# Kernel optimization log

Hardware: AMD Instinct MI355X
Metric: run time of the kernel (lower is better)

## Reference

```python
import jax, jax.numpy as jnp
import numpy as np

B = 1024      # batch
DIN = 103     # generator/encoder input dim
L1, L2 = 64, 32   # encoder layer widths (latent = 32)
E = 8         # NUM_EXPERTS
GH = 64       # gating hidden width
H = 256       # generator hidden width
DOUT = 51     # generator output dim
EPS = 1e-5    # BatchNorm eps


def setup_inputs() -> dict:
    key = jax.random.key(0)
    ks = jax.random.split(key, 24)
    s = 0.05
    f32 = jnp.float32
    return {
        "x": jax.random.normal(ks[0], (B, DIN), f32),
        # encoder Linear + BN params
        "w1": jax.random.normal(ks[1], (L1, DIN), f32) * s,
        "b1": jnp.zeros((L1,), f32),
        "gamma1": jnp.ones((L1,), f32),
        "beta1": jnp.zeros((L1,), f32),
        "w2": jax.random.normal(ks[2], (L2, L1), f32) * s,
        "b2": jnp.zeros((L2,), f32),
        "gamma2": jnp.ones((L2,), f32),
        "beta2": jnp.zeros((L2,), f32),
        # gating MLP (latent 32 -> GH -> GH -> E, ELU, softmax)
        "gw1": jax.random.normal(ks[3], (GH, L2), f32) * s,
        "gb1": jnp.zeros((GH,), f32),
        "gw2": jax.random.normal(ks[4], (GH, GH), f32) * s,
        "gb2": jnp.zeros((GH,), f32),
        "gw3": jax.random.normal(ks[5], (E, GH), f32) * s,
        "gb3": jnp.zeros((E,), f32),
        # expert weight banks for 3-layer generator (MANN style)
        "ew1": jax.random.normal(ks[6], (E, DIN, H), f32) * s,
        "eb1": jnp.zeros((E, H), f32),
        "ew2": jax.random.normal(ks[7], (E, H, H), f32) * s,
        "eb2": jnp.zeros((E, H), f32),
        "ew3": jax.random.normal(ks[8], (E, H, DOUT), f32) * s,
        "eb3": jnp.zeros((E, DOUT), f32),
    }


def _batchnorm(h, gamma, beta):
    # training-mode BatchNorm1d: per-batch mean/var (biased var, matching torch)
    m = jnp.mean(h, axis=0)
    v = jnp.mean((h - m) ** 2, axis=0)
    return gamma * (h - m) * jax.lax.rsqrt(v + EPS) + beta


def reference(x, w1, b1, gamma1, beta1, w2, b2, gamma2, beta2,
              gw1, gb1, gw2, gb2, gw3, gb3,
              ew1, eb1, ew2, eb2, ew3, eb3):
    # in-place scale of last 3 features (x[:,100:103] *= 100)
    xs = x.at[:, 100:103].multiply(100.0)
    # encoder: Linear -> BN -> ReLU, twice
    h = jax.nn.relu(_batchnorm(xs @ w1.T + b1, gamma1, beta1))
    latent = jax.nn.relu(_batchnorm(h @ w2.T + b2, gamma2, beta2))
    # gating network -> blending coefficients BC [B, E]
    g = jax.nn.elu(latent @ gw1.T + gb1)
    g = jax.nn.elu(g @ gw2.T + gb2)
    bc = jax.nn.softmax(g @ gw3.T + gb3, axis=-1)
    # MANN-style generator: per-sample expert-blended weights
    wb1 = jnp.einsum('be,eih->bih', bc, ew1)   # [B, DIN, H]
    h1 = jax.nn.elu(jnp.einsum('bi,bih->bh', xs, wb1) + bc @ eb1)
    wb2 = jnp.einsum('be,ehk->bhk', bc, ew2)   # [B, H, H]
    h2 = jax.nn.elu(jnp.einsum('bh,bhk->bk', h1, wb2) + bc @ eb2)
    wb3 = jnp.einsum('be,eho->bho', bc, ew3)   # [B, H, DOUT]
    out = jnp.einsum('bh,bho->bo', h2, wb3) + bc @ eb3
    return out
```

## Files before the change

### kernel.cpp

```cpp
#include <hip/hip_runtime.h>
#include <math.h>


#define DIN 103
#define NE  8
#define HH  256
#define DOUT 51
#define EPSBN 1e-5f

typedef __attribute__((ext_vector_type(8))) short bf16x8;
typedef __attribute__((ext_vector_type(4))) float f32x4;
typedef __attribute__((ext_vector_type(8))) unsigned short us8;
typedef unsigned short ushort_t;

__device__ __forceinline__ float eluf(float v) { return v > 0.f ? v : (expf(v) - 1.f); }
__device__ __forceinline__ unsigned short bf16h(float f) {
  unsigned u = __float_as_uint(f);
  u += 0x7FFFu + ((u >> 16) & 1u);
  return (unsigned short)(u >> 16);
}
__device__ __forceinline__ float bf16f(unsigned short h) { return __uint_as_float(((unsigned)h) << 16); }
__device__ __forceinline__ void split_bf16(float v, unsigned short& h, unsigned short& l) {
  h = bf16h(v);
  l = bf16h(v - bf16f(h));
}
#define MFMA __builtin_amdgcn_mfma_f32_16x16x32_bf16

__device__ __forceinline__ void stA(float* p, float v) {
  __hip_atomic_store(p, v, __ATOMIC_RELAXED, __HIP_MEMORY_SCOPE_AGENT);
}
__device__ __forceinline__ float ldA(const float* p) {
  return __hip_atomic_load((float*)p, __ATOMIC_RELAXED, __HIP_MEMORY_SCOPE_AGENT);
}
__device__ __forceinline__ void stAu(unsigned* p, unsigned v) {
  __hip_atomic_store(p, v, __ATOMIC_RELAXED, __HIP_MEMORY_SCOPE_AGENT);
}
__device__ __forceinline__ unsigned ldAu(const unsigned* p) {
  return __hip_atomic_load((unsigned*)p, __ATOMIC_RELAXED, __HIP_MEMORY_SCOPE_AGENT);
}

#define O_SLOTS1 0
#define O_SLOTS2 8192
#define O_H1RAW  20480
#define O_XSH    118784
#define O_XSL    184320
#define O_E1H    258048
#define O_E1L    389120
#define O_E2H    520192
#define O_E3H    782336
#define O_ESPAN  589824
#define O_BAR    1372160

__device__ __forceinline__ void gbar64(unsigned* base, int blk) {
  asm volatile("s_waitcnt vmcnt(0)" ::: "memory");
  __syncthreads();
  if (threadIdx.x == 0) {
    unsigned a = __hip_atomic_fetch_add(base + (blk >> 3) * 32, 1u,
                                        __ATOMIC_RELAXED, __HIP_MEMORY_SCOPE_AGENT);
    if (a == 7u) {
      unsigned r = __hip_atomic_fetch_add(base + 256, 1u,
                                          __ATOMIC_RELAXED, __HIP_MEMORY_SCOPE_AGENT);
      if (r == 7u) {
#pragma unroll
        for (int j = 0; j < 8; ++j) stAu(base + 288 + j * 32, 1u);
      }
    }
    while (ldAu(base + 288 + (blk & 7) * 32) == 0u)
      __builtin_amdgcn_s_sleep(2);
  }
  __syncthreads();
}

__global__ __launch_bounds__(256) void k_prep_enc1(
    const float* __restrict__ x, const float* __restrict__ w1, const float* __restrict__ b1,
    const float* __restrict__ ew1, const float* __restrict__ ew2, const float* __restrict__ ew3,
    float* __restrict__ ws) {
  __shared__ union {
    float tile[32][65];
    float xt[16][104];
    struct { float w1L[64 * DIN]; float xr[16][104]; float hb[16][64]; } e1;
  } sm;
  int bk = blockIdx.x, t = threadIdx.x;
  int l2 = t & 63, c = l2 & 15, q = l2 >> 4;
  if (bk == 0) {
    unsigned* bz = (unsigned*)(ws + O_BAR);
#pragma unroll
    for (int i = 0; i < 4; ++i) bz[t + i * 256] = 0u;
  }

  if (bk < 256) {
    int nh = bk & 3, kc = (bk >> 2) & 7, e = bk >> 5;
    int k0 = kc * 32, n0 = nh * 64;
#pragma unroll
    for (int i = 0; i < 8; ++i) {
      int kl = (t >> 6) + i * 4;
      sm.tile[kl][t & 63] = ew2[((size_t)e * HH + k0 + kl) * HH + n0 + (t & 63)];
    }
    __syncthreads();
    int nsl = t >> 6;
    us8 H8;
#pragma unroll
    for (int j = 0; j < 8; ++j) H8[j] = bf16h(sm.tile[q * 8 + j][nsl * 16 + c]);
    size_t dst = (((size_t)(e * 16 + nh * 4 + nsl)) * 8 + kc) * 512 + l2 * 8;
    *(us8*)((ushort_t*)(ws + O_E2H) + dst) = H8;
  } else if (bk < 384) {
    int b2 = bk - 256;
    int nh = b2 & 3, kc = (b2 >> 2) & 3, e = b2 >> 4;
    int k0 = kc * 32, n0 = nh * 64;
#pragma unroll
    for (int i = 0; i < 8; ++i) {
      int kl = (t >> 6) + i * 4;
      int k = k0 + kl;
      sm.tile[kl][t & 63] = (k < DIN) ? ew1[((size_t)e * DIN + k) * HH + n0 + (t & 63)] : 0.f;
    }
    __syncthreads();
    int nsl = t >> 6;
    us8 H8, L8;
#pragma unroll
    for (int j = 0; j < 8; ++j) {
      unsigned short h, lo; split_bf16(sm.tile[q * 8 + j][nsl * 16 + c], h, lo);
      H8[j] = h; L8[j] = lo;
    }
    size_t dst = (((size_t)(e * 16 + nh * 4 + nsl)) * 4 + kc) * 512 + l2 * 8;
    *(us8*)((ushort_t*)(ws + O_E1H) + dst) = H8;
    *(us8*)((ushort_t*)(ws + O_E1L) + dst) = L8;
  } else if (bk < 448) {
    int b2 = bk - 384;
    int kc = b2 & 7, e = b2 >> 3;
    int k0 = kc * 32;
#pragma unroll
    for (int i = 0; i < 8; ++i) {
      int kl = (t >> 6) + i * 4;
      int n = t & 63;
      sm.tile[kl][n] = (n < DOUT) ? ew3[((size_t)e * HH + k0 + kl) * DOUT + n] : 0.f;
    }
    __syncthreads();
    int nsl = t >> 6;
    us8 H8;
#pragma unroll
    for (int j = 0; j < 8; ++j) H8[j] = bf16h(sm.tile[q * 8 + j][nsl * 16 + c]);
    size_t dst = (((size_t)(e * 4 + nsl)) * 8 + kc) * 512 + l2 * 8;
    *(us8*)((ushort_t*)(ws + O_E3H) + dst) = H8;
  } else if (bk < 512) {
    int msub = bk - 448;
    for (int i = t; i < 16 * 104; i += 256) {
      int b = i / 104, k = i - b * 104;
      float v = 0.f;
      if (k < DIN) { v = x[(size_t)(msub * 16 + b) * DIN + k]; if (k >= 100) v *= 100.f; }
      sm.xt[b][k] = v;
    }
    __syncthreads();
    int kc = t >> 6;
    int m = c;
    us8 H8, L8;
#pragma unroll
    for (int j = 0; j < 8; ++j) {
      int k = kc * 32 + q * 8 + j;
      float v = (k < 104) ? sm.xt[m][k] : 0.f;
      unsigned short h, lo; split_bf16(v, h, lo);
      H8[j] = h; L8[j] = lo;
    }
    size_t dst = ((size_t)msub * 4 + kc) * 512 + l2 * 8;
    *(us8*)((ushort_t*)(ws + O_XSH) + dst) = H8;
    *(us8*)((ushort_t*)(ws + O_XSL) + dst) = L8;
  } else {
    float* slots1 = ws + O_SLOTS1;
    float* h1raw  = ws + O_H1RAW;
    int bkl = bk - 512;
    int r0 = bkl * 16;
    for (int i = t; i < 64 * DIN; i += 256) sm.e1.w1L[i] = w1[i];
    for (int i = t; i < 16 * 104; i += 256) {
      int r = i / 104, c2 = i - r * 104;
      float v = 0.f;
      if (c2 < DIN) { v = x[(size_t)(r0 + r) * DIN + c2]; if (c2 >= 100) v *= 100.f; }
      sm.e1.xr[r][c2] = v;
    }
    __syncthreads();
#pragma unroll
    for (int i = 0; i < 4; ++i) {
      int idx = t + i * 256;
      int r = idx >> 6, j = idx & 63;
      float acc = b1[j];
      for (int k = 0; k < DIN; ++k) acc = fmaf(sm.e1.xr[r][k], sm.e1.w1L[j * DIN + k], acc);
      sm.e1.hb[r][j] = acc;
      h1raw[(size_t)(r0 + r) * 64 + j] = acc;
    }
    __syncthreads();
    if (t < 64) {
      float s = 0.f, qq = 0.f;
      for (int r = 0; r < 16; ++r) { float v = sm.e1.hb[r][t]; s += v; qq += v * v; }
      slots1[bkl * 128 + t] = s;
      slots1[bkl * 128 + 64 + t] = qq;
    }
  }
}

__global__ __launch_bounds__(512) void k_mega(
    const float* __restrict__ gamma1, const float* __restrict__ beta1,
    const float* __restrict__ w2, const float* __restrict__ b2,
    const float* __restrict__ gamma2, const float* __restrict__ beta2,
    const float* __restrict__ gw1, const float* __restrict__ gb1,
    const float* __restrict__ gw2, const float* __restrict__ gb2,
    const float* __restrict__ gw3, const float* __restrict__ gb3,
    const float* __restrict__ eb1, const float* __restrict__ eb2,
    const float* __restrict__ eb3,
    float* __restrict__ ws, float* __restrict__ out) {
  __shared__ union {
    struct { float w2T[64 * 33]; float red[128]; float sc1[64], sh1[64];
             float h1b[16][64]; } enc2;
    struct { float gw1L[64 * 33]; float gw2L[64 * 65]; float gw3L[8 * 65];
             float gb1L[64], gb2L[64], gb3L[8];
             float red2[64], sc2[32], sh2[32];
             float lat[16][32]; float g1[16][64], g2[16][64]; } gate;
    struct { float hT[256][17]; float eb[2048]; } comb;
    struct { float p3s[8][16][64]; float eb3L[8][64]; } g3;
  } U;
  __shared__ float hb2s[16][32];
  __shared__ us8 aHv[512], aLv[512];
  __shared__ float bcL[16][8];

  const int blk = blockIdx.x, t = threadIdx.x;
  const int wv = t >> 6, l = t & 63, c = l & 15, quad = l >> 4;
  const int R0 = blk * 16;
  unsigned* bar = (unsigned*)(ws + O_BAR);
  const ushort_t* XsH = (const ushort_t*)(ws + O_XSH);
  const ushort_t* XsL = (const ushort_t*)(ws + O_XSL);
  const ushort_t* E1H = (const ushort_t*)(ws + O_E1H);
  const ushort_t* E1L = (const ushort_t*)(ws + O_E1L);
  const ushort_t* E2H = (const ushort_t*)(ws + O_E2H);
  const ushort_t* E3H = (const ushort_t*)(ws + O_E3H);

  bf16x8 a1h[4], a1l[4];
#pragma unroll
  for (int kc = 0; kc < 4; ++kc) {
    a1h[kc] = *(const bf16x8*)(XsH + ((size_t)blk * 4 + kc) * 512 + l * 8);
    a1l[kc] = *(const bf16x8*)(XsL + ((size_t)blk * 4 + kc) * 512 + l * 8);
  }

  {
    const int slice = blk >> 3;
    const float4* src = (const float4*)(ws + O_E1H);
    float ka = 0.f;
#pragma unroll
    for (int i = 0; i < 36; ++i) {
      float4 v = src[(size_t)slice * 18432 + (size_t)i * 512 + t];
      ka += v.x + v.y + v.z + v.w;
    }
    asm volatile("" :: "v"(ka));
  }

  {
    const float* slots1 = ws + O_SLOTS1;
    float* slots2 = ws + O_SLOTS2;
    const float* h1raw = ws + O_H1RAW;
    for (int i = t; i < 2048; i += 512) { int j = i >> 6, k = i & 63; U.enc2.w2T[k * 33 + j] = w2[i]; }
    if (t < 128) {
      float s = 0.f;
      for (int b = 0; b < 64; ++b) s += slots1[b * 128 + t];
      U.enc2.red[t] = s;
    }
    __syncthreads();
    if (t < 64) {
      float mm = U.enc2.red[t] * (1.f / 1024.f);
      float v = U.enc2.red[64 + t] * (1.f / 1024.f) - mm * mm;
      float sc = gamma1[t] * rsqrtf(v + EPSBN);
      U.enc2.sc1[t] = sc; U.enc2.sh1[t] = beta1[t] - mm * sc;
    }
    __syncthreads();
#pragma unroll
    for (int i = 0; i < 2; ++i) {
      int idx = t + i * 512;
      int r = idx >> 6, k = idx & 63;
      U.enc2.h1b[r][k] = fmaxf(fmaf(h1raw[(size_t)(R0 + r) * 64 + k], U.enc2.sc1[k], U.enc2.sh1[k]), 0.f);
    }
    __syncthreads();
    {
      int r = t >> 5, j = t & 31;
      float acc = b2[j];
      for (int k = 0; k < 64; ++k) acc = fmaf(U.enc2.h1b[r][k], U.enc2.w2T[k * 33 + j], acc);
      hb2s[r][j] = acc;
    }
    __syncthreads();
    if (t < 32) {
      float s = 0.f, q = 0.f;
      for (int r = 0; r < 16; ++r) { float v = hb2s[r][t]; s += v; q += v * v; }
      stA(slots2 + blk * 64 + t, s);
      stA(slots2 + blk * 64 + 32 + t, q);
    }
  }
  gbar64(bar, blk);

  {
    const float* slots2 = ws + O_SLOTS2;
    for (int i = t; i < 2048; i += 512) { int j = i >> 5, k = i & 31; U.gate.gw1L[j * 33 + k] = gw1[i]; }
    for (int i = t; i < 4096; i += 512) { int j = i >> 6, k = i & 63; U.gate.gw2L[j * 65 + k] = gw2[i]; }
    { int j = t >> 6, k = t & 63; U.gate.gw3L[j * 65 + k] = gw3[t]; }
    if (t < 64) { U.gate.gb1L[t] = gb1[t]; U.gate.gb2L[t] = gb2[t]; }
    if (t < 8) U.gate.gb3L[t] = gb3[t];
    if (t < 64) {
      float vvv[64];
#pragma unroll
      for (int b = 0; b < 64; ++b) vvv[b] = ldA(slots2 + b * 64 + t);
      float s = 0.f;
#pragma unroll
      for (int b = 0; b < 64; ++b) s += vvv[b];
      U.gate.red2[t] = s;
    }
    __syncthreads();
    if (t < 32) {
      float mm = U.gate.red2[t] * (1.f / 1024.f);
      float v = U.gate.red2[32 + t] * (1.f / 1024.f) - mm * mm;
      float sc = gamma2[t] * rsqrtf(v + EPSBN);
      U.gate.sc2[t] = sc; U.gate.sh2[t] = beta2[t] - mm * sc;
    }
    __syncthreads();
    { int r = t >> 5, cc = t & 31;
      U.gate.lat[r][cc] = fmaxf(fmaf(hb2s[r][cc], U.gate.sc2[cc], U.gate.sh2[cc]), 0.f); }
    __syncthreads();
#pragma unroll
    for (int rr = 0; rr < 2; ++rr) {
      int r = wv * 2 + rr;
      float a1 = U.gate.gb1L[l];
      for (int k = 0; k < 32; ++k) a1 = fmaf(U.gate.gw1L[l * 33 + k], U.gate.lat[r][k], a1);
      U.gate.g1[r][l] = eluf(a1);
    }
    __syncthreads();
#pragma unroll
    for (int rr = 0; rr < 2; ++rr) {
      int r = wv * 2 + rr;
      float a2 = U.gate.gb2L[l];
      for (int k = 0; k < 64; ++k) a2 = fmaf(U.gate.gw2L[l * 65 + k], U.gate.g1[r][k], a2);
      U.gate.g2[r][l] = eluf(a2);
    }
    __syncthreads();
#pragma unroll
    for (int rr = 0; rr < 2; ++rr) {
      int r = wv * 2 + rr;
      if (l < 8) {
        float a3 = U.gate.gb3L[l];
        for (int k = 0; k < 64; ++k) a3 = fmaf(U.gate.gw3L[l * 65 + k], U.gate.g2[r][k], a3);
        float mx = a3;
        mx = fmaxf(mx, __shfl_xor(mx, 1));
        mx = fmaxf(mx, __shfl_xor(mx, 2));
        mx = fmaxf(mx, __shfl_xor(mx, 4));
        float p = expf(a3 - mx);
        float sp = p;
        sp += __shfl_xor(sp, 1); sp += __shfl_xor(sp, 2); sp += __shfl_xor(sp, 4);
        bcL[r][l] = p / sp;
      }
    }
    __syncthreads();

    for (int i = t; i < 2048; i += 512) U.comb.eb[i] = eb1[i];
    __syncthreads();
    {
      f32x4 blend[2] = {};
#pragma unroll
      for (int e = 0; e < NE; ++e) {
        float bcv[4];
#pragma unroll
        for (int r = 0; r < 4; ++r) bcv[r] = bcL[quad * 4 + r][e];
#pragma unroll
        for (int nsi = 0; nsi < 2; ++nsi) {
          int ns = wv * 2 + nsi;
          f32x4 acc = {};
#pragma unroll
          for (int kc = 0; kc < 4; ++kc) {
            size_t bo = (((size_t)(e * 16 + ns)) * 4 + kc) * 512 + l * 8;
            bf16x8 bh = *(const bf16x8*)(E1H + bo);
            bf16x8 bl = *(const bf16x8*)(E1L + bo);
            acc = MFMA(a1h[kc], bh, acc, 0, 0, 0);
            acc = MFMA(a1l[kc], bh, acc, 0, 0, 0);
            acc = MFMA(a1h[kc], bl, acc, 0, 0, 0);
          }
          float ebv = U.comb.eb[e * HH + ns * 16 + c];
#pragma unroll
          for (int r = 0; r < 4; ++r) blend[nsi][r] = fmaf(bcv[r], acc[r] + ebv, blend[nsi][r]);
        }
      }
#pragma unroll
      for (int nsi = 0; nsi < 2; ++nsi) {
        int col = (wv * 2 + nsi) * 16 + c;
#pragma unroll
        for (int r = 0; r < 4; ++r) U.comb.hT[col][quad * 4 + r] = eluf(blend[nsi][r]);
      }
    }
    __syncthreads();
    {
      int l2 = t & 63, row = l2 & 15, k0 = (t >> 6) * 32 + (l2 >> 4) * 8;
      us8 H, L;
#pragma unroll
      for (int j = 0; j < 8; ++j) {
        unsigned short h, lo; split_bf16(U.comb.hT[k0 + j][row], h, lo);
        H[j] = h; L[j] = lo;
      }
      aHv[t] = H; aLv[t] = L;
    }
    __syncthreads();
  }

  {
    for (int i = t; i < 2048; i += 512) U.comb.eb[i] = eb2[i];
    bf16x8 a2h[8], a2l[8];
#pragma unroll
    for (int kc = 0; kc < 8; ++kc) {
      a2h[kc] = *(const bf16x8*)&aHv[kc * 64 + l];
      a2l[kc] = *(const bf16x8*)&aLv[kc * 64 + l];
    }
    __syncthreads();
    {
      f32x4 blend[2] = {};
#pragma unroll
      for (int e = 0; e < NE; ++e) {
        float bcv[4];
#pragma unroll
        for (int r = 0; r < 4; ++r) bcv[r] = bcL[quad * 4 + r][e];
#pragma unroll
        for (int nsi = 0; nsi < 2; ++nsi) {
          int ns = wv * 2 + nsi;
          f32x4 acc = {};
#pragma unroll
          for (int kc = 0; kc < 8; ++kc) {
            size_t bo = (((size_t)(e * 16 + ns)) * 8 + kc) * 512 + l * 8;
            bf16x8 bh = *(const bf16x8*)(E2H + bo);
            acc = MFMA(a2h[kc], bh, acc, 0, 0, 0);
            acc = MFMA(a2l[kc], bh, acc, 0, 0, 0);
          }
          float ebv = U.comb.eb[e * HH + ns * 16 + c];
#pragma unroll
          for (int r = 0; r < 4; ++r) blend[nsi][r] = fmaf(bcv[r], acc[r] + ebv, blend[nsi][r]);
        }
      }
#pragma unroll
      for (int nsi = 0; nsi < 2; ++nsi) {
        int col = (wv * 2 + nsi) * 16 + c;
#pragma unroll
        for (int r = 0; r < 4; ++r) U.comb.hT[col][quad * 4 + r] = eluf(blend[nsi][r]);
      }
    }
    __syncthreads();
    {
      int l2 = t & 63, row = l2 & 15, k0 = (t >> 6) * 32 + (l2 >> 4) * 8;
      us8 H, L;
#pragma unroll
      for (int j = 0; j < 8; ++j) {
        unsigned short h, lo; split_bf16(U.comb.hT[k0 + j][row], h, lo);
        H[j] = h; L[j] = lo;
      }
      aHv[t] = H; aLv[t] = L;
    }
    __syncthreads();
  }

  {
    { int e = t >> 6, n = t & 63; U.g3.eb3L[e][n] = (n < DOUT) ? eb3[e * DOUT + n] : 0.f; }
    const int e = wv;
    f32x4 acc[4] = {};
#pragma unroll
    for (int kc = 0; kc < 8; ++kc) {
      bf16x8 ah = *(const bf16x8*)&aHv[kc * 64 + l];
      bf16x8 al = *(const bf16x8*)&aLv[kc * 64 + l];
#pragma unroll
      for (int nsi = 0; nsi < 4; ++nsi) {
        size_t bo = (((size_t)(e * 4 + nsi)) * 8 + kc) * 512 + l * 8;
        bf16x8 bh = *(const bf16x8*)(E3H + bo);
        acc[nsi] = MFMA(ah, bh, acc[nsi], 0, 0, 0);
        acc[nsi] = MFMA(al, bh, acc[nsi], 0, 0, 0);
      }
    }
#pragma unroll
    for (int nsi = 0; nsi < 4; ++nsi)
#pragma unroll
      for (int r = 0; r < 4; ++r)
        U.g3.p3s[e][quad * 4 + r][nsi * 16 + c] = acc[nsi][r];
    __syncthreads();
#pragma unroll
    for (int i = 0; i < 2; ++i) {
      int idx = t + i * 512;
      int row = idx >> 6, col = idx & 63;
      float s = 0.f;
#pragma unroll
      for (int e2 = 0; e2 < 8; ++e2)
        s = fmaf(bcL[row][e2], U.g3.p3s[e2][row][col] + U.g3.eb3L[e2][col], s);
      if (col < DOUT) out[(size_t)(R0 + row) * DOUT + col] = s;
    }
  }
}

extern "C" void kernel_launch(void* const* d_in, const int* in_sizes, int n_in,
                              void* d_out, int out_size, void* d_ws, size_t ws_size,
                              hipStream_t stream) {
  const float* x      = (const float*)d_in[0];
  const float* w1     = (const float*)d_in[1];
  const float* b1     = (const float*)d_in[2];
  const float* gamma1 = (const float*)d_in[3];
  const float* beta1  = (const float*)d_in[4];
  const float* w2     = (const float*)d_in[5];
  const float* b2     = (const float*)d_in[6];
  const float* gamma2 = (const float*)d_in[7];
  const float* beta2  = (const float*)d_in[8];
  const float* gw1    = (const float*)d_in[9];
  const float* gb1    = (const float*)d_in[10];
  const float* gw2    = (const float*)d_in[11];
  const float* gb2    = (const float*)d_in[12];
  const float* gw3    = (const float*)d_in[13];
  const float* gb3    = (const float*)d_in[14];
  const float* ew1    = (const float*)d_in[15];
  const float* eb1    = (const float*)d_in[16];
  const float* ew2    = (const float*)d_in[17];
  const float* eb2    = (const float*)d_in[18];
  const float* ew3    = (const float*)d_in[19];
  const float* eb3    = (const float*)d_in[20];
  float* wsf  = (float*)d_ws;
  float* outp = (float*)d_out;

  k_prep_enc1<<<576, 256, 0, stream>>>(x, w1, b1, ew1, ew2, ew3, wsf);
  k_mega<<<64, 512, 0, stream>>>(gamma1, beta1, w2, b2, gamma2, beta2,
                                 gw1, gb1, gw2, gb2, gw3, gb3,
                                 eb1, eb2, eb3, wsf, outp);
}
```

Before: 151.2 us.

## Double k_mega block to 1024 threads, one wave per output column tile

Launches the persistent mega-kernel with 1024 threads (16 waves) per block instead of 512, and reassigns work so that each wave handles one 16-column tile in the layer-1 and layer-2 blended MFMA loops instead of two. The gating MLP now gives one row per wave, and the layer-3 expert MFMAs are restricted to the first 8 waves. The aim is more latency hiding and parallelism within each of the 64 blocks on a grid that is otherwise small. In exchange, register pressure is higher at 1024 launch bounds, and the A-operand fragments for layer 2 are reloaded from memory inside the loop rather than kept in registers.

Result: faster. 141.9 us (-6.1%).

```diff
diff --git a/kernel.cpp b/kernel.cpp
--- a/kernel.cpp
+++ b/kernel.cpp
@@ -48,7 +48,6 @@
 #define O_E1L    389120
 #define O_E2H    520192
 #define O_E3H    782336
-#define O_ESPAN  589824
 #define O_BAR    1372160
 
 __device__ __forceinline__ void gbar64(unsigned* base, int blk) {
@@ -195,7 +194,7 @@
   }
 }
 
-__global__ __launch_bounds__(512) void k_mega(
+__global__ __launch_bounds__(1024) void k_mega(
     const float* __restrict__ gamma1, const float* __restrict__ beta1,
     const float* __restrict__ w2, const float* __restrict__ b2,
     const float* __restrict__ gamma2, const float* __restrict__ beta2,
@@ -242,8 +241,8 @@
     const float4* src = (const float4*)(ws + O_E1H);
     float ka = 0.f;
 #pragma unroll
-    for (int i = 0; i < 36; ++i) {
-      float4 v = src[(size_t)slice * 18432 + (size_t)i * 512 + t];
+    for (int i = 0; i < 18; ++i) {
+      float4 v = src[(size_t)slice * 18432 + (size_t)i * 1024 + t];
       ka += v.x + v.y + v.z + v.w;
     }
     asm volatile("" :: "v"(ka));
@@ -253,7 +252,7 @@
     const float* slots1 = ws + O_SLOTS1;
     float* slots2 = ws + O_SLOTS2;
     const float* h1raw = ws + O_H1RAW;
-    for (int i = t; i < 2048; i += 512) { int j = i >> 6, k = i & 63; U.enc2.w2T[k * 33 + j] = w2[i]; }
+    for (int i = t; i < 2048; i += 1024) { int j = i >> 6, k = i & 63; U.enc2.w2T[k * 33 + j] = w2[i]; }
     if (t < 128) {
       float s = 0.f;
       for (int b = 0; b < 64; ++b) s += slots1[b * 128 + t];
@@ -267,14 +266,10 @@
       U.enc2.sc1[t] = sc; U.enc2.sh1[t] = beta1[t] - mm * sc;
     }
     __syncthreads();
-#pragma unroll
-    for (int i = 0; i < 2; ++i) {
-      int idx = t + i * 512;
-      int r = idx >> 6, k = idx & 63;
-      U.enc2.h1b[r][k] = fmaxf(fmaf(h1raw[(size_t)(R0 + r) * 64 + k], U.enc2.sc1[k], U.enc2.sh1[k]), 0.f);
-    }
-    __syncthreads();
-    {
+    { int r = t >> 6, k = t & 63;
+      U.enc2.h1b[r][k] = fmaxf(fmaf(h1raw[(size_t)(R0 + r) * 64 + k], U.enc2.sc1[k], U.enc2.sh1[k]), 0.f); }
+    __syncthreads();
+    if (t < 512) {
       int r = t >> 5, j = t & 31;
       float acc = b2[j];
       for (int k = 0; k < 64; ++k) acc = fmaf(U.enc2.h1b[r][k], U.enc2.w2T[k * 33 + j], acc);
@@ -292,9 +287,9 @@
 
   {
     const float* slots2 = ws + O_SLOTS2;
-    for (int i = t; i < 2048; i += 512) { int j = i >> 5, k = i & 31; U.gate.gw1L[j * 33 + k] = gw1[i]; }
-    for (int i = t; i < 4096; i += 512) { int j = i >> 6, k = i & 63; U.gate.gw2L[j * 65 + k] = gw2[i]; }
-    { int j = t >> 6, k = t & 63; U.gate.gw3L[j * 65 + k] = gw3[t]; }
+    for (int i = t; i < 2048; i += 1024) { int j = i >> 5, k = i & 31; U.gate.gw1L[j * 33 + k] = gw1[i]; }
+    for (int i = t; i < 4096; i += 1024) { int j = i >> 6, k = i & 63; U.gate.gw2L[j * 65 + k] = gw2[i]; }
+    if (t < 512) { int j = t >> 6, k = t & 63; U.gate.gw3L[j * 65 + k] = gw3[t]; }
     if (t < 64) { U.gate.gb1L[t] = gb1[t]; U.gate.gb2L[t] = gb2[t]; }
     if (t < 8) U.gate.gb3L[t] = gb3[t];
     if (t < 64) {
@@ -314,28 +309,22 @@
       U.gate.sc2[t] = sc; U.gate.sh2[t] = beta2[t] - mm * sc;
     }
     __syncthreads();
-    { int r = t >> 5, cc = t & 31;
+    if (t < 512) { int r = t >> 5, cc = t & 31;
       U.gate.lat[r][cc] = fmaxf(fmaf(hb2s[r][cc], U.gate.sc2[cc], U.gate.sh2[cc]), 0.f); }
     __syncthreads();
-#pragma unroll
-    for (int rr = 0; rr < 2; ++rr) {
-      int r = wv * 2 + rr;
+    { int r = wv;
       float a1 = U.gate.gb1L[l];
       for (int k = 0; k < 32; ++k) a1 = fmaf(U.gate.gw1L[l * 33 + k], U.gate.lat[r][k], a1);
       U.gate.g1[r][l] = eluf(a1);
     }
     __syncthreads();
-#pragma unroll
-    for (int rr = 0; rr < 2; ++rr) {
-      int r = wv * 2 + rr;
+    { int r = wv;
       float a2 = U.gate.gb2L[l];
       for (int k = 0; k < 64; ++k) a2 = fmaf(U.gate.gw2L[l * 65 + k], U.gate.g1[r][k], a2);
       U.gate.g2[r][l] = eluf(a2);
     }
     __syncthreads();
-#pragma unroll
-    for (int rr = 0; rr < 2; ++rr) {
-      int r = wv * 2 + rr;
+    { int r = wv;
       if (l < 8) {
         float a3 = U.gate.gb3L[l];
         for (int k = 0; k < 64; ++k) a3 = fmaf(U.gate.gw3L[l * 65 + k], U.gate.g2[r][k], a3);
@@ -351,42 +340,36 @@
     }
     __syncthreads();
 
-    for (int i = t; i < 2048; i += 512) U.comb.eb[i] = eb1[i];
+    for (int i = t; i < 2048; i += 1024) U.comb.eb[i] = eb1[i];
     __syncthreads();
     {
-      f32x4 blend[2] = {};
+      const int ns = wv;
+      f32x4 blend = {};
 #pragma unroll
       for (int e = 0; e < NE; ++e) {
         float bcv[4];
 #pragma unroll
         for (int r = 0; r < 4; ++r) bcv[r] = bcL[quad * 4 + r][e];
-#pragma unroll
-        for (int nsi = 0; nsi < 2; ++nsi) {
-          int ns = wv * 2 + nsi;
-          f32x4 acc = {};
-#pragma unroll
-          for (int kc = 0; kc < 4; ++kc) {
-            size_t bo = (((size_t)(e * 16 + ns)) * 4 + kc) * 512 + l * 8;
-            bf16x8 bh = *(const bf16x8*)(E1H + bo);
-            bf16x8 bl = *(const bf16x8*)(E1L + bo);
-            acc = MFMA(a1h[kc], bh, acc, 0, 0, 0);
-            acc = MFMA(a1l[kc], bh, acc, 0, 0, 0);
-            acc = MFMA(a1h[kc], bl, acc, 0, 0, 0);
-          }
-          float ebv = U.comb.eb[e * HH + ns * 16 + c];
-#pragma unroll
-          for (int r = 0; r < 4; ++r) blend[nsi][r] = fmaf(bcv[r], acc[r] + ebv, blend[nsi][r]);
+        f32x4 acc = {};
+#pragma unroll
+        for (int kc = 0; kc < 4; ++kc) {
+          size_t bo = (((size_t)(e * 16 + ns)) * 4 + kc) * 512 + l * 8;
+          bf16x8 bh = *(const bf16x8*)(E1H + bo);
+          bf16x8 bl = *(const bf16x8*)(E1L + bo);
+          acc = MFMA(a1h[kc], bh, acc, 0, 0, 0);
+          acc = MFMA(a1l[kc], bh, acc, 0, 0, 0);
+          acc = MFMA(a1h[kc], bl, acc, 0, 0, 0);
         }
-      }
-#pragma unroll
-      for (int nsi = 0; nsi < 2; ++nsi) {
-        int col = (wv * 2 + nsi) * 16 + c;
-#pragma unroll
-        for (int r = 0; r < 4; ++r) U.comb.hT[col][quad * 4 + r] = eluf(blend[nsi][r]);
-      }
-    }
-    __syncthreads();
-    {
+        float ebv = U.comb.eb[e * HH + ns * 16 + c];
+#pragma unroll
+        for (int r = 0; r < 4; ++r) blend[r] = fmaf(bcv[r], acc[r] + ebv, blend[r]);
+      }
+      int col = ns * 16 + c;
+#pragma unroll
+      for (int r = 0; r < 4; ++r) U.comb.hT[col][quad * 4 + r] = eluf(blend[r]);
+    }
+    __syncthreads();
+    if (t < 512) {
       int l2 = t & 63, row = l2 & 15, k0 = (t >> 6) * 32 + (l2 >> 4) * 8;
       us8 H, L;
 #pragma unroll
@@ -400,46 +383,36 @@
   }
 
   {
-    for (int i = t; i < 2048; i += 512) U.comb.eb[i] = eb2[i];
-    bf16x8 a2h[8], a2l[8];
-#pragma unroll
-    for (int kc = 0; kc < 8; ++kc) {
-      a2h[kc] = *(const bf16x8*)&aHv[kc * 64 + l];
-      a2l[kc] = *(const bf16x8*)&aLv[kc * 64 + l];
-    }
+    for (int i = t; i < 2048; i += 1024) U.comb.eb[i] = eb2[i];
     __syncthreads();
     {
-      f32x4 blend[2] = {};
+      const int ns = wv;
+      f32x4 blend = {};
 #pragma unroll
       for (int e = 0; e < NE; ++e) {
         float bcv[4];
 #pragma unroll
         for (int r = 0; r < 4; ++r) bcv[r] = bcL[quad * 4 + r][e];
-#pragma unroll
-        for (int nsi = 0; nsi < 2; ++nsi) {
-          int ns = wv * 2 + nsi;
-          f32x4 acc = {};
-#pragma unroll
-          for (int kc = 0; kc < 8; ++kc) {
-            size_t bo = (((size_t)(e * 16 + ns)) * 8 + kc) * 512 + l * 8;
-            bf16x8 bh = *(const bf16x8*)(E2H + bo);
-            acc = MFMA(a2h[kc], bh, acc, 0, 0, 0);
-            acc = MFMA(a2l[kc], bh, acc, 0, 0, 0);
-          }
-          float ebv = U.comb.eb[e * HH + ns * 16 + c];
-#pragma unroll
-          for (int r = 0; r < 4; ++r) blend[nsi][r] = fmaf(bcv[r], acc[r] + ebv, blend[nsi][r]);
+        f32x4 acc = {};
+#pragma unroll
+        for (int kc = 0; kc < 8; ++kc) {
+          size_t bo = (((size_t)(e * 16 + ns)) * 8 + kc) * 512 + l * 8;
+          bf16x8 bh = *(const bf16x8*)(E2H + bo);
+          bf16x8 ah = *(const bf16x8*)&aHv[kc * 64 + l];
+          bf16x8 al = *(const bf16x8*)&aLv[kc * 64 + l];
+          acc = MFMA(ah, bh, acc, 0, 0, 0);
+          acc = MFMA(al, bh, acc, 0, 0, 0);
         }
-      }
-#pragma unroll
-      for (int nsi = 0; nsi < 2; ++nsi) {
-        int col = (wv * 2 + nsi) * 16 + c;
-#pragma unroll
-        for (int r = 0; r < 4; ++r) U.comb.hT[col][quad * 4 + r] = eluf(blend[nsi][r]);
-      }
-    }
-    __syncthreads();
-    {
+        float ebv = U.comb.eb[e * HH + ns * 16 + c];
+#pragma unroll
+        for (int r = 0; r < 4; ++r) blend[r] = fmaf(bcv[r], acc[r] + ebv, blend[r]);
+      }
+      int col = ns * 16 + c;
+#pragma unroll
+      for (int r = 0; r < 4; ++r) U.comb.hT[col][quad * 4 + r] = eluf(blend[r]);
+    }
+    __syncthreads();
+    if (t < 512) {
       int l2 = t & 63, row = l2 & 15, k0 = (t >> 6) * 32 + (l2 >> 4) * 8;
       us8 H, L;
 #pragma unroll
@@ -453,31 +426,31 @@
   }
 
   {
-    { int e = t >> 6, n = t & 63; U.g3.eb3L[e][n] = (n < DOUT) ? eb3[e * DOUT + n] : 0.f; }
-    const int e = wv;
-    f32x4 acc[4] = {};
-#pragma unroll
-    for (int kc = 0; kc < 8; ++kc) {
-      bf16x8 ah = *(const bf16x8*)&aHv[kc * 64 + l];
-      bf16x8 al = *(const bf16x8*)&aLv[kc * 64 + l];
-#pragma unroll
-      for (int nsi = 0; nsi < 4; ++nsi) {
-        size_t bo = (((size_t)(e * 4 + nsi)) * 8 + kc) * 512 + l * 8;
-        bf16x8 bh = *(const bf16x8*)(E3H + bo);
-        acc[nsi] = MFMA(ah, bh, acc[nsi], 0, 0, 0);
-        acc[nsi] = MFMA(al, bh, acc[nsi], 0, 0, 0);
-      }
-    }
-#pragma unroll
-    for (int nsi = 0; nsi < 4; ++nsi)
-#pragma unroll
-      for (int r = 0; r < 4; ++r)
-        U.g3.p3s[e][quad * 4 + r][nsi * 16 + c] = acc[nsi][r];
-    __syncthreads();
-#pragma unroll
-    for (int i = 0; i < 2; ++i) {
-      int idx = t + i * 512;
-      int row = idx >> 6, col = idx & 63;
+    if (t < 512) { int e = t >> 6, n = t & 63; U.g3.eb3L[e][n] = (n < DOUT) ? eb3[e * DOUT + n] : 0.f; }
+    if (wv < 8) {
+      const int e = wv;
+      f32x4 acc[4] = {};
+#pragma unroll
+      for (int kc = 0; kc < 8; ++kc) {
+        bf16x8 ah = *(const bf16x8*)&aHv[kc * 64 + l];
+        bf16x8 al = *(const bf16x8*)&aLv[kc * 64 + l];
+#pragma unroll
+        for (int nsi = 0; nsi < 4; ++nsi) {
+          size_t bo = (((size_t)(e * 4 + nsi)) * 8 + kc) * 512 + l * 8;
+          bf16x8 bh = *(const bf16x8*)(E3H + bo);
+          acc[nsi] = MFMA(ah, bh, acc[nsi], 0, 0, 0);
+          acc[nsi] = MFMA(al, bh, acc[nsi], 0, 0, 0);
+        }
+      }
+#pragma unroll
+      for (int nsi = 0; nsi < 4; ++nsi)
+#pragma unroll
+        for (int r = 0; r < 4; ++r)
+          U.g3.p3s[e][quad * 4 + r][nsi * 16 + c] = acc[nsi][r];
+    }
+    __syncthreads();
+    {
+      int row = t >> 6, col = t & 63;
       float s = 0.f;
 #pragma unroll
       for (int e2 = 0; e2 < 8; ++e2)
@@ -515,7 +488,7 @@
   float* outp = (float*)d_out;
 
   k_prep_enc1<<<576, 256, 0, stream>>>(x, w1, b1, ew1, ew2, ew3, wsf);
-  k_mega<<<64, 512, 0, stream>>>(gamma1, beta1, w2, b2, gamma2, beta2,
-                                 gw1, gb1, gw2, gb2, gw3, gb3,
-                                 eb1, eb2, eb3, wsf, outp);
-}
+  k_mega<<<64, 1024, 0, stream>>>(gamma1, beta1, w2, b2, gamma2, beta2,
+                                  gw1, gb1, gw2, gb2, gw3, gb3,
+                                  eb1, eb2, eb3, wsf, outp);
+}
```

## Split generator layers across block groups with LDS-staged expert weights and grid barriers

Applied to the files above, without the earlier changes.

Each block used to compute all 256 hidden columns for its own 16 rows and read every expert weight tile straight from global memory. Now groups of four blocks share 64 rows. Each block computes one 64-column slice, and the expert weight tiles for that slice are staged in LDS once per expert and reused by all waves. Layer 1 and 2 activations, plus the blend coefficients, are exchanged through workspace buffers with three extra grid barriers. This cuts per-block weight traffic and drops the old L2 prefetch warm-up loop, at the cost of more grid-wide synchronisation and global round trips for activations.

Result: slower. 193.2 us (+27.8%).

```diff
diff --git a/kernel.cpp b/kernel.cpp
--- a/kernel.cpp
+++ b/kernel.cpp
@@ -38,9 +38,24 @@
 __device__ __forceinline__ unsigned ldAu(const unsigned* p) {
   return __hip_atomic_load((unsigned*)p, __ATOMIC_RELAXED, __HIP_MEMORY_SCOPE_AGENT);
 }
+union U16B { us8 v; bf16x8 b; unsigned u[4]; };
+__device__ __forceinline__ void st16A(void* p, us8 x) {
+  U16B t; t.v = x;
+  unsigned* d = (unsigned*)p;
+#pragma unroll
+  for (int j = 0; j < 4; ++j) stAu(d + j, t.u[j]);
+}
+__device__ __forceinline__ bf16x8 ld16A(const void* p) {
+  U16B t;
+  const unsigned* s = (const unsigned*)p;
+#pragma unroll
+  for (int j = 0; j < 4; ++j) t.u[j] = ldAu(s + j);
+  return t.b;
+}
 
 #define O_SLOTS1 0
 #define O_SLOTS2 8192
+#define O_BCG    12288
 #define O_H1RAW  20480
 #define O_XSH    118784
 #define O_XSL    184320
@@ -48,7 +63,10 @@
 #define O_E1L    389120
 #define O_E2H    520192
 #define O_E3H    782336
-#define O_ESPAN  589824
+#define O_A1H    847872
+#define O_A1L    978944
+#define O_A2H    1110016
+#define O_A2L    1241088
 #define O_BAR    1372160
 
 __device__ __forceinline__ void gbar64(unsigned* base, int blk) {
@@ -82,8 +100,8 @@
   } sm;
   int bk = blockIdx.x, t = threadIdx.x;
   int l2 = t & 63, c = l2 & 15, q = l2 >> 4;
-  if (bk == 0) {
-    unsigned* bz = (unsigned*)(ws + O_BAR);
+  if (bk < 4) {
+    unsigned* bz = (unsigned*)(ws + O_BAR) + bk * 1024;
 #pragma unroll
     for (int i = 0; i < 4; ++i) bz[t + i * 256] = 0u;
   }
@@ -212,41 +230,38 @@
              float gb1L[64], gb2L[64], gb3L[8];
              float red2[64], sc2[32], sh2[32];
              float lat[16][32]; float g1[16][64], g2[16][64]; } gate;
-    struct { float hT[256][17]; float eb[2048]; } comb;
+    struct { ushort_t stage[32 * 512]; float hT4[4][64][17]; float ebs[512]; } gen;
     struct { float p3s[8][16][64]; float eb3L[8][64]; } g3;
   } U;
   __shared__ float hb2s[16][32];
-  __shared__ us8 aHv[512], aLv[512];
-  __shared__ float bcL[16][8];
+  __shared__ float bc4L[4][16][8];
+  __shared__ float bcL2[16][8];
 
   const int blk = blockIdx.x, t = threadIdx.x;
   const int wv = t >> 6, l = t & 63, c = l & 15, quad = l >> 4;
-  const int R0 = blk * 16;
+  const int msub = blk;
+  const int R0 = msub * 16;
+  const int mg = blk >> 2, g = blk & 3;
+  const int ml = wv >> 1, nsp = wv & 1;
+  const int m_w = mg * 4 + ml;
   unsigned* bar = (unsigned*)(ws + O_BAR);
+  float* bcg = ws + O_BCG;
   const ushort_t* XsH = (const ushort_t*)(ws + O_XSH);
   const ushort_t* XsL = (const ushort_t*)(ws + O_XSL);
   const ushort_t* E1H = (const ushort_t*)(ws + O_E1H);
   const ushort_t* E1L = (const ushort_t*)(ws + O_E1L);
   const ushort_t* E2H = (const ushort_t*)(ws + O_E2H);
   const ushort_t* E3H = (const ushort_t*)(ws + O_E3H);
+  ushort_t* A1Hp = (ushort_t*)(ws + O_A1H);
+  ushort_t* A1Lp = (ushort_t*)(ws + O_A1L);
+  ushort_t* A2Hp = (ushort_t*)(ws + O_A2H);
+  ushort_t* A2Lp = (ushort_t*)(ws + O_A2L);
 
   bf16x8 a1h[4], a1l[4];
 #pragma unroll
   for (int kc = 0; kc < 4; ++kc) {
-    a1h[kc] = *(const bf16x8*)(XsH + ((size_t)blk * 4 + kc) * 512 + l * 8);
-    a1l[kc] = *(const bf16x8*)(XsL + ((size_t)blk * 4 + kc) * 512 + l * 8);
-  }
-
-  {
-    const int slice = blk >> 3;
-    const float4* src = (const float4*)(ws + O_E1H);
-    float ka = 0.f;
-#pragma unroll
-    for (int i = 0; i < 36; ++i) {
-      float4 v = src[(size_t)slice * 18432 + (size_t)i * 512 + t];
-      ka += v.x + v.y + v.z + v.w;
-    }
-    asm volatile("" :: "v"(ka));
+    a1h[kc] = *(const bf16x8*)(XsH + ((size_t)m_w * 4 + kc) * 512 + l * 8);
+    a1l[kc] = *(const bf16x8*)(XsL + ((size_t)m_w * 4 + kc) * 512 + l * 8);
   }
 
   {
@@ -284,8 +299,8 @@
     if (t < 32) {
       float s = 0.f, q = 0.f;
       for (int r = 0; r < 16; ++r) { float v = hb2s[r][t]; s += v; q += v * v; }
-      stA(slots2 + blk * 64 + t, s);
-      stA(slots2 + blk * 64 + 32 + t, q);
+      stA(slots2 + msub * 64 + t, s);
+      stA(slots2 + msub * 64 + 32 + t, q);
     }
   }
   gbar64(bar, blk);
@@ -346,126 +361,150 @@
         float p = expf(a3 - mx);
         float sp = p;
         sp += __shfl_xor(sp, 1); sp += __shfl_xor(sp, 2); sp += __shfl_xor(sp, 4);
-        bcL[r][l] = p / sp;
-      }
-    }
-    __syncthreads();
-
-    for (int i = t; i < 2048; i += 512) U.comb.eb[i] = eb1[i];
+        float bcv = p / sp;
+        bcL2[r][l] = bcv;
+        stA(bcg + (size_t)(R0 + r) * 8 + l, bcv);
+      }
+    }
+  }
+  gbar64(bar + 1024, blk);
+
+  {
+    { int mli = t >> 7, r = (t >> 3) & 15, e = t & 7;
+      bc4L[mli][r][e] = ldA(bcg + ((size_t)(mg * 4 + mli) * 16 + r) * 8 + e); }
+    { U.gen.ebs[t] = eb1[(t >> 6) * HH + g * 64 + (t & 63)]; }
+    f32x4 blend[2] = {};
+    for (int e = 0; e < 8; ++e) {
+      __syncthreads();
+#pragma unroll
+      for (int i = 0; i < 4; ++i) {
+        int s = wv * 4 + i;
+        int hl = s >> 4, nsl = (s >> 2) & 3, kc = s & 3;
+        const ushort_t* src = (hl ? E1L : E1H) + (((size_t)(e * 16 + g * 4 + nsl) * 4 + kc) * 512) + l * 8;
+        *(us8*)(U.gen.stage + s * 512 + l * 8) = *(const us8*)src;
+      }
+      __syncthreads();
+      float bcv[4];
+#pragma unroll
+      for (int r = 0; r < 4; ++r) bcv[r] = bc4L[ml][quad * 4 + r][e];
+#pragma unroll
+      for (int nsi = 0; nsi < 2; ++nsi) {
+        int nsl = nsp * 2 + nsi;
+        f32x4 acc = {};
+#pragma unroll
+        for (int kc = 0; kc < 4; ++kc) {
+          bf16x8 bh = *(const bf16x8*)(U.gen.stage + (size_t)((nsl * 4 + kc)) * 512 + l * 8);
+          bf16x8 bl = *(const bf16x8*)(U.gen.stage + (size_t)((16 + nsl * 4 + kc)) * 512 + l * 8);
+          acc = MFMA(a1h[kc], bh, acc, 0, 0, 0);
+          acc = MFMA(a1l[kc], bh, acc, 0, 0, 0);
+          acc = MFMA(a1h[kc], bl, acc, 0, 0, 0);
+        }
+        float ebv = U.gen.ebs[e * 64 + nsl * 16 + c];
+#pragma unroll
+        for (int r = 0; r < 4; ++r) blend[nsi][r] = fmaf(bcv[r], acc[r] + ebv, blend[nsi][r]);
+      }
+    }
+#pragma unroll
+    for (int nsi = 0; nsi < 2; ++nsi) {
+      int col = (nsp * 2 + nsi) * 16 + c;
+#pragma unroll
+      for (int r = 0; r < 4; ++r) U.gen.hT4[ml][col][quad * 4 + r] = eluf(blend[nsi][r]);
+    }
     __syncthreads();
     {
-      f32x4 blend[2] = {};
-#pragma unroll
-      for (int e = 0; e < NE; ++e) {
-        float bcv[4];
-#pragma unroll
-        for (int r = 0; r < 4; ++r) bcv[r] = bcL[quad * 4 + r][e];
-#pragma unroll
-        for (int nsi = 0; nsi < 2; ++nsi) {
-          int ns = wv * 2 + nsi;
-          f32x4 acc = {};
-#pragma unroll
-          for (int kc = 0; kc < 4; ++kc) {
-            size_t bo = (((size_t)(e * 16 + ns)) * 4 + kc) * 512 + l * 8;
-            bf16x8 bh = *(const bf16x8*)(E1H + bo);
-            bf16x8 bl = *(const bf16x8*)(E1L + bo);
-            acc = MFMA(a1h[kc], bh, acc, 0, 0, 0);
-            acc = MFMA(a1l[kc], bh, acc, 0, 0, 0);
-            acc = MFMA(a1h[kc], bl, acc, 0, 0, 0);
-          }
-          float ebv = U.comb.eb[e * HH + ns * 16 + c];
-#pragma unroll
-          for (int r = 0; r < 4; ++r) blend[nsi][r] = fmaf(bcv[r], acc[r] + ebv, blend[nsi][r]);
+      int mli = t >> 7, kcl = (t >> 6) & 1, l2 = t & 63, row = l2 & 15;
+      int k0l = kcl * 32 + (l2 >> 4) * 8;
+      us8 H, L;
+#pragma unroll
+      for (int j = 0; j < 8; ++j) {
+        unsigned short h, lo; split_bf16(U.gen.hT4[mli][k0l + j][row], h, lo);
+        H[j] = h; L[j] = lo;
+      }
+      size_t dst = ((size_t)(mg * 4 + mli) * 8 + g * 2 + kcl) * 512 + l2 * 8;
+      st16A(A1Hp + dst, H);
+      st16A(A1Lp + dst, L);
+    }
+  }
+  gbar64(bar + 2048, blk);
+
+  {
+    bf16x8 ah[8], al[8];
+#pragma unroll
+    for (int kc = 0; kc < 8; ++kc) {
+      ah[kc] = ld16A(A1Hp + ((size_t)m_w * 8 + kc) * 512 + l * 8);
+      al[kc] = ld16A(A1Lp + ((size_t)m_w * 8 + kc) * 512 + l * 8);
+    }
+    { U.gen.ebs[t] = eb2[(t >> 6) * HH + g * 64 + (t & 63)]; }
+    f32x4 blend[2] = {};
+    for (int e = 0; e < 8; ++e) {
+      __syncthreads();
+#pragma unroll
+      for (int i = 0; i < 4; ++i) {
+        int s = wv * 4 + i;
+        int nsl = s >> 3, kc = s & 7;
+        const ushort_t* src = E2H + (((size_t)(e * 16 + g * 4 + nsl) * 8 + kc) * 512) + l * 8;
+        *(us8*)(U.gen.stage + s * 512 + l * 8) = *(const us8*)src;
+      }
+      __syncthreads();
+      float bcv[4];
+#pragma unroll
+      for (int r = 0; r < 4; ++r) bcv[r] = bc4L[ml][quad * 4 + r][e];
+#pragma unroll
+      for (int nsi = 0; nsi < 2; ++nsi) {
+        int nsl = nsp * 2 + nsi;
+        f32x4 acc = {};
+#pragma unroll
+        for (int kc = 0; kc < 8; ++kc) {
+          bf16x8 bh = *(const bf16x8*)(U.gen.stage + (size_t)(nsl * 8 + kc) * 512 + l * 8);
+          acc = MFMA(ah[kc], bh, acc, 0, 0, 0);
+          acc = MFMA(al[kc], bh, acc, 0, 0, 0);
         }
-      }
-#pragma unroll
-      for (int nsi = 0; nsi < 2; ++nsi) {
-        int col = (wv * 2 + nsi) * 16 + c;
-#pragma unroll
-        for (int r = 0; r < 4; ++r) U.comb.hT[col][quad * 4 + r] = eluf(blend[nsi][r]);
-      }
+        float ebv = U.gen.ebs[e * 64 + nsl * 16 + c];
+#pragma unroll
+        for (int r = 0; r < 4; ++r) blend[nsi][r] = fmaf(bcv[r], acc[r] + ebv, blend[nsi][r]);
+      }
+    }
+#pragma unroll
+    for (int nsi = 0; nsi < 2; ++nsi) {
+      int col = (nsp * 2 + nsi) * 16 + c;
+#pragma unroll
+      for (int r = 0; r < 4; ++r) U.gen.hT4[ml][col][quad * 4 + r] = eluf(blend[nsi][r]);
     }
     __syncthreads();
     {
-      int l2 = t & 63, row = l2 & 15, k0 = (t >> 6) * 32 + (l2 >> 4) * 8;
+      int mli = t >> 7, kcl = (t >> 6) & 1, l2 = t & 63, row = l2 & 15;
+      int k0l = kcl * 32 + (l2 >> 4) * 8;
       us8 H, L;
 #pragma unroll
       for (int j = 0; j < 8; ++j) {
-        unsigned short h, lo; split_bf16(U.comb.hT[k0 + j][row], h, lo);
+        unsigned short h, lo; split_bf16(U.gen.hT4[mli][k0l + j][row], h, lo);
         H[j] = h; L[j] = lo;
       }
-      aHv[t] = H; aLv[t] = L;
-    }
-    __syncthreads();
-  }
-
-  {
-    for (int i = t; i < 2048; i += 512) U.comb.eb[i] = eb2[i];
-    bf16x8 a2h[8], a2l[8];
-#pragma unroll
-    for (int kc = 0; kc < 8; ++kc) {
-      a2h[kc] = *(const bf16x8*)&aHv[kc * 64 + l];
-      a2l[kc] = *(const bf16x8*)&aLv[kc * 64 + l];
-    }
-    __syncthreads();
-    {
-      f32x4 blend[2] = {};
-#pragma unroll
-      for (int e = 0; e < NE; ++e) {
-        float bcv[4];
-#pragma unroll
-        for (int r = 0; r < 4; ++r) bcv[r] = bcL[quad * 4 + r][e];
-#pragma unroll
-        for (int nsi = 0; nsi < 2; ++nsi) {
-          int ns = wv * 2 + nsi;
-          f32x4 acc = {};
-#pragma unroll
-          for (int kc = 0; kc < 8; ++kc) {
-            size_t bo = (((size_t)(e * 16 + ns)) * 8 + kc) * 512 + l * 8;
-            bf16x8 bh = *(const bf16x8*)(E2H + bo);
-            acc = MFMA(a2h[kc], bh, acc, 0, 0, 0);
-            acc = MFMA(a2l[kc], bh, acc, 0, 0, 0);
-          }
-          float ebv = U.comb.eb[e * HH + ns * 16 + c];
-#pragma unroll
-          for (int r = 0; r < 4; ++r) blend[nsi][r] = fmaf(bcv[r], acc[r] + ebv, blend[nsi][r]);
-        }
-      }
-#pragma unroll
-      for (int nsi = 0; nsi < 2; ++nsi) {
-        int col = (wv * 2 + nsi) * 16 + c;
-#pragma unroll
-        for (int r = 0; r < 4; ++r) U.comb.hT[col][quad * 4 + r] = eluf(blend[nsi][r]);
-      }
-    }
-    __syncthreads();
-    {
-      int l2 = t & 63, row = l2 & 15, k0 = (t >> 6) * 32 + (l2 >> 4) * 8;
-      us8 H, L;
-#pragma unroll
-      for (int j = 0; j < 8; ++j) {
-        unsigned short h, lo; split_bf16(U.comb.hT[k0 + j][row], h, lo);
-        H[j] = h; L[j] = lo;
-      }
-      aHv[t] = H; aLv[t] = L;
-    }
-    __syncthreads();
-  }
+      size_t dst = ((size_t)(mg * 4 + mli) * 8 + g * 2 + kcl) * 512 + l2 * 8;
+      st16A(A2Hp + dst, H);
+      st16A(A2Lp + dst, L);
+    }
+  }
+  gbar64(bar + 3072, blk);
 
   {
     { int e = t >> 6, n = t & 63; U.g3.eb3L[e][n] = (n < DOUT) ? eb3[e * DOUT + n] : 0.f; }
+    bf16x8 ah[8], al[8];
+#pragma unroll
+    for (int kc = 0; kc < 8; ++kc) {
+      ah[kc] = ld16A(A2Hp + ((size_t)msub * 8 + kc) * 512 + l * 8);
+      al[kc] = ld16A(A2Lp + ((size_t)msub * 8 + kc) * 512 + l * 8);
+    }
     const int e = wv;
     f32x4 acc[4] = {};
 #pragma unroll
     for (int kc = 0; kc < 8; ++kc) {
-      bf16x8 ah = *(const bf16x8*)&aHv[kc * 64 + l];
-      bf16x8 al = *(const bf16x8*)&aLv[kc * 64 + l];
 #pragma unroll
       for (int nsi = 0; nsi < 4; ++nsi) {
         size_t bo = (((size_t)(e * 4 + nsi)) * 8 + kc) * 512 + l * 8;
         bf16x8 bh = *(const bf16x8*)(E3H + bo);
-        acc[nsi] = MFMA(ah, bh, acc[nsi], 0, 0, 0);
-        acc[nsi] = MFMA(al, bh, acc[nsi], 0, 0, 0);
+        acc[nsi] = MFMA(ah[kc], bh, acc[nsi], 0, 0, 0);
+        acc[nsi] = MFMA(al[kc], bh, acc[nsi], 0, 0, 0);
       }
     }
 #pragma unroll
@@ -481,7 +520,7 @@
       float s = 0.f;
 #pragma unroll
       for (int e2 = 0; e2 < 8; ++e2)
-        s = fmaf(bcL[row][e2], U.g3.p3s[e2][row][col] + U.g3.eb3L[e2][col], s);
+        s = fmaf(bcL2[row][e2], U.g3.p3s[e2][row][col] + U.g3.eb3L[e2][col], s);
       if (col < DOUT) out[(size_t)(R0 + row) * DOUT + col] = s;
     }
   }
```
